# Kernel tuning notes

Hardware: AMD Instinct MI355X
Metric: run time of the kernel (lower is better)

The kernel has to match this reference:

```python
import jax, jax.numpy as jnp
from jax import lax
import numpy as np

EPS = 1e-5

def sign_ste(x):
    # Binarize to {-1,+1} with straight-through estimator (matches BNN Binarize)
    return x + lax.stop_gradient(jnp.where(x >= 0, 1.0, -1.0).astype(x.dtype) - x)

def bn(x, g, b, m, v, axis):
    shp = [1] * x.ndim
    shp[axis] = -1
    inv = g.reshape(shp) / jnp.sqrt(v.reshape(shp) + EPS)
    return (x - m.reshape(shp)) * inv + b.reshape(shp)

def bconv(x, w, b, p):
    # binarized-weight conv, NCHW / OIHW
    y = lax.conv_general_dilated(x, sign_ste(w), (1, 1), [(p, p), (p, p)],
                                 dimension_numbers=('NCHW', 'OIHW', 'NCHW'))
    return y + b[None, :, None, None]

def conv_block(x, w, b, g, bt, m, v, p):
    # BinarizeConv2d -> BatchNorm2d(eval) -> Hardtanh -> Quantizer(1 bit)
    return sign_ste(jnp.clip(bn(bconv(x, w, b, p), g, bt, m, v, 1), -1.0, 1.0))

def maxpool2(x):
    return lax.reduce_window(x, -jnp.inf, lax.max, (1, 1, 2, 2), (1, 1, 2, 2), 'VALID')


def setup_inputs() -> dict:
    key = jax.random.key(0)
    ks = iter(jax.random.split(key, 64))
    B = 4096
    d = {}
    d['x'] = jax.random.normal(next(ks), (B, 1, 28, 28), dtype=jnp.float32)

    def u(shape):
        return jax.random.uniform(next(ks), shape, minval=-1.0, maxval=1.0, dtype=jnp.float32)

    def bn_params(c, pre):
        d[pre + 'g'] = u((c,)) * 0.5 + 1.0
        d[pre + 'bt'] = u((c,)) * 0.1
        d[pre + 'm'] = u((c,)) * 0.1
        d[pre + 'v'] = jax.random.uniform(next(ks), (c,), minval=0.5, maxval=1.5, dtype=jnp.float32)

    # stem conv 1->16, k=3
    d['w1'] = u((16, 1, 3, 3)); d['b1'] = jnp.full((16,), 0.01, jnp.float32); bn_params(16, '')
    d['g1'], d['bt1'], d['m1'], d['v1'] = d.pop('g'), d.pop('bt'), d.pop('m'), d.pop('v')
    # inception branches 16->32 each
    d['wa'] = u((32, 16, 1, 1)); d['ba'] = jnp.full((32,), 0.01, jnp.float32); bn_params(32, 'a_')
    d['wb'] = u((32, 16, 3, 3)); d['bb'] = jnp.full((32,), 0.01, jnp.float32); bn_params(32, 'b_')
    d['wc'] = u((32, 16, 5, 5)); d['bc'] = jnp.full((32,), 0.01, jnp.float32); bn_params(32, 'c_')
    # classifier
    d['wf1'] = u((1024, 7 * 7 * 3 * 32)); d['bf1'] = jnp.full((1024,), 0.01, jnp.float32); bn_params(1024, 'f1_')
    d['wf2'] = u((10, 1024)); d['bf2'] = jnp.full((10,), 0.01, jnp.float32); bn_params(10, 'f2_')
    return d


def reference(x, w1, b1, g1, bt1, m1, v1,
              wa, ba, a_g, a_bt, a_m, a_v,
              wb, bb, b_g, b_bt, b_m, b_v,
              wc, bc, c_g, c_bt, c_m, c_v,
              wf1, bf1, f1_g, f1_bt, f1_m, f1_v,
              wf2, bf2, f2_g, f2_bt, f2_m, f2_v):
    h = conv_block(x, w1, b1, g1, bt1, m1, v1, 1)          # [B,16,28,28]
    h = maxpool2(h)                                         # [B,16,14,14]
    h = sign_ste(h)  # BinarizeConv2d binarizes its input (>1 channel); no-op on +/-1
    ya = conv_block(h, wa, ba, a_g, a_bt, a_m, a_v, 0)
    yb = conv_block(h, wb, bb, b_g, b_bt, b_m, b_v, 1)
    yc = conv_block(h, wc, bc, c_g, c_bt, c_m, c_v, 2)
    h = jnp.concatenate([ya, yb, yc], axis=1)               # [B,96,14,14]
    h = maxpool2(h)                                         # [B,96,7,7]
    h = h.reshape(h.shape[0], -1)                           # [B,4704] (NCHW flatten)
    # fc1: binarized input + binarized weights, BN1d, hardtanh, quantize
    h = sign_ste(h) @ sign_ste(wf1).T + bf1
    h = sign_ste(jnp.clip(bn(h, f1_g, f1_bt, f1_m, f1_v, 1), -1.0, 1.0))
    # dropout is identity in eval mode
    h = sign_ste(h) @ sign_ste(wf2).T + bf2
    h = bn(h, f2_g, f2_bt, f2_m, f2_v, 1)
    return jax.nn.log_softmax(h, axis=-1)                   # [B,10]
```

## Files before the change

kernel.cpp:

```cpp
#include <hip/hip_runtime.h>
#include <stdint.h>

typedef unsigned long long u64;
typedef unsigned int u32;
typedef unsigned short u16;

struct InPtrs { const float* p[37]; };

#define OFF_THR1     0
#define OFF_W1D      128
#define OFF_WREC     1280
#define OFF_SMAXBC   4352
#define OFF_SMAXF1   11008
#define OFF_WF2P     15104
#define OFF_A2       16384
#define OFF_C2       16448
#define OFF_WF1P     16512
#define OFF_H2       622720
#define OFF_HB2      3047552

__device__ __forceinline__ int clampi(int v, int lo, int hi) { return v < lo ? lo : (v > hi ? hi : v); }

__global__ __launch_bounds__(1024) void kprep(InPtrs P, char* __restrict__ ws) {
  const float* w1 = P.p[1]; const float* b1 = P.p[2];
  const float* g1 = P.p[3]; const float* bt1 = P.p[4]; const float* m1 = P.p[5]; const float* v1 = P.p[6];
  const float* wa = P.p[7]; const float* ba = P.p[8];
  const float* ag = P.p[9]; const float* abt = P.p[10]; const float* am = P.p[11]; const float* av = P.p[12];
  const float* wb = P.p[13]; const float* bb = P.p[14];
  const float* bg = P.p[15]; const float* bbt = P.p[16]; const float* bm = P.p[17]; const float* bv = P.p[18];
  const float* wc = P.p[19]; const float* bc = P.p[20];
  const float* bf1 = P.p[26];
  const float* f1g = P.p[27]; const float* f1bt = P.p[28]; const float* f1m = P.p[29]; const float* f1v = P.p[30];
  const float* wf2 = P.p[31]; const float* bf2 = P.p[32];
  const float* cg = P.p[21]; const float* cbt = P.p[22]; const float* cm = P.p[23]; const float* cv = P.p[24];
  const float* f2g = P.p[33]; const float* f2bt = P.p[34]; const float* f2m = P.p[35]; const float* f2v = P.p[36];

  double* thr1 = (double*)(ws + OFF_THR1);
  double* w1d  = (double*)(ws + OFF_W1D);
  u64* wrec = (u64*)(ws + OFF_WREC);
  u64* smaxbc = (u64*)(ws + OFF_SMAXBC);
  int* smf1 = (int*)(ws + OFF_SMAXF1);
  u64* wf2p = (u64*)(ws + OFF_WF2P);
  float* a2 = (float*)(ws + OFF_A2);
  float* c2 = (float*)(ws + OFF_C2);

  __shared__ u64 wbpL[96];
  __shared__ u64 wcpL[256];
  __shared__ double thBL[32], thCL[32];
  __shared__ u32 wamS[32], smaS[32];

  int t = threadIdx.x;
  int wave = t >> 6, lane = t & 63;
  int blk = blockIdx.x;

  if (blk == 0) {
    if (t < 32) {
      u32 m = 0;
      for (int c = 0; c < 16; c++) if (wa[t*16+c] >= 0.f) m |= 1u << c;
      wamS[t] = m;
      double ia = (double)ag[t] / sqrt((double)av[t] + 1e-5);
      double thA = (double)am[t] - (double)abt[t]/ia - (double)ba[t];
      int kmin = (int)ceil(thA);
      int sm = (16 - kmin) >> 1;
      smaS[t] = (u32)clampi(sm + 1, 0, 65535);
      double ib = (double)bg[t] / sqrt((double)bv[t] + 1e-5);
      thBL[t] = (double)bm[t] - (double)bbt[t]/ib - (double)bb[t];
      double ic = (double)cg[t] / sqrt((double)cv[t] + 1e-5);
      thCL[t] = (double)cm[t] - (double)cbt[t]/ic - (double)bc[t];
    }
    for (int w = wave; w < 96; w += 16) {
      int ch = w / 3, k = w - 3*ch;
      int tt = 4*k + (lane >> 4), c = lane & 15;
      bool pred = false;
      if (tt < 9) pred = (wb[ch*144 + c*9 + tt] >= 0.f);
      u64 m = __ballot(pred);
      if (lane == 0) wbpL[w] = m;
    }
    for (int w = wave; w < 256; w += 16) {
      int ch = w >> 3, k = w & 7;
      int tt = 4*k + (lane >> 4), c = lane & 15;
      bool pred = false;
      if (k < 7 && tt < 25) pred = (wc[ch*400 + c*25 + tt] >= 0.f);
      u64 m = __ballot(pred);
      if (lane == 0) wcpL[w] = m;
    }
    __syncthreads();
    if (t < 384) {
      int ch = t / 12, k = t - 12*ch;
      u64 v = 0;
      if (k < 7) v = wcpL[ch*8 + k];
      else if (k < 10) v = wbpL[ch*3 + (k - 7)];
      wrec[ch*12 + k] = v;
    }
    if (t < 800) {
      const int irep[5] = {0, 1, 5, 12, 13};
      int cls = t >> 5, ch = t & 31;
      int rc = cls / 5, cc = cls - 5*rc;
      int ir = irep[rc], jr = irep[cc];
      u64 invC[7] = {0,0,0,0,0,0,0};
      u64 invB[3] = {0,0,0};
      int nInvC = 0, nInvB = 0;
      #pragma unroll
      for (int tt = 0; tt < 25; tt++) {
        int di = tt/5 - 2, dj = tt%5 - 2;
        bool val = (ir+di >= 0 && ir+di < 14 && jr+dj >= 0 && jr+dj < 14);
        if (!val) { invC[tt>>2] |= 0xFFFFull << ((tt&3)*16); nInvC++; }
      }
      #pragma unroll
      for (int tt = 0; tt < 9; tt++) {
        int di = tt/3 - 1, dj = tt%3 - 1;
        bool val = (ir+di >= 0 && ir+di < 14 && jr+dj >= 0 && jr+dj < 14);
        if (!val) { invB[tt>>2] |= 0xFFFFull << ((tt&3)*16); nInvB++; }
      }
      int pinvC = 0;
      #pragma unroll
      for (int k = 0; k < 7; k++) pinvC += __popcll(wcpL[ch*8+k] & invC[k]);
      int pinvB = 0;
      #pragma unroll
      for (int k = 0; k < 3; k++) pinvB += __popcll(wbpL[ch*3+k] & invB[k]);
      int nvC = 16*(25 - nInvC), nvB = 16*(9 - nInvB);
      int kminC = (int)ceil(thCL[ch]);
      int kminB = (int)ceil(thBL[ch]);
      int smC = ((nvC - kminC) >> 1) + pinvC;
      int smB = ((nvB - kminB) >> 1) + pinvB;
      u64 pB = (u64)clampi(smB + 1, 0, 65535);
      u64 pC = (u64)clampi(smC + 1, 0, 65535);
      smaxbc[cls*33 + ch] = ((u64)wamS[ch] << 48) | ((u64)smaS[ch] << 32) | (pB << 16) | pC;
    }
  } else if (blk == 1) {
    for (int w = wave; w < 160; w += 16) {
      int o = w >> 4, kk = w & 15;
      bool pred = (wf2[o*1024 + kk*64 + lane] >= 0.f);
      u64 m = __ballot(pred);
      if (lane == 0) wf2p[w] = m;
    }
  } else if (blk == 2) {
    {
      int o = t;
      double inv = (double)f1g[o] / sqrt((double)f1v[o] + 1e-5);
      double th = (double)f1m[o] - (double)f1bt[o]/inv - (double)bf1[o];
      int kmin = (int)ceil(th);
      smf1[o] = ((4704 - kmin) >> 1) + 1;
    }
    if (t < 10) {
      double inv = (double)f2g[t] / sqrt((double)f2v[t] + 1e-5);
      a2[t] = (float)inv;
      c2[t] = (float)(((double)bf2[t] - (double)f2m[t]) * inv + (double)f2bt[t]);
    }
  } else {
    if (t < 144) w1d[t] = (w1[t] >= 0.f) ? 1.0 : -1.0;
    if (t < 16) {
      double inv = (double)g1[t] / sqrt((double)v1[t] + 1e-5);
      thr1[t] = (double)m1[t] - (double)bt1[t] / inv - (double)b1[t];
    }
  }
}

__global__ __launch_bounds__(256) void kfused(const float* __restrict__ x, const float* __restrict__ wf1,
                                              const char* __restrict__ ws,
                                              u32* __restrict__ h2u32, u64* __restrict__ wf1p) {
  __shared__ float wshF[144];
  __shared__ float thrF[16];
  __shared__ double thrD[16];
  __shared__ u16 hp[324];
  __shared__ u32 rr[196][3];
  __shared__ u64 smbc[825];
  __shared__ __align__(16) u64 wrecL[384];

  int t = threadIdx.x;

  if (blockIdx.x < 1024) {
    unsigned char* flag = (unsigned char*)smbc;
    int o = blockIdx.x;
    const float* row = wf1 + (size_t)o*4704;
    for (int i = t; i < 4704; i += 256) flag[i] = (row[i] >= 0.f);
    __syncthreads();
    int w0 = t >> 6, lane = t & 63;
    for (int w = w0; w < 74; w += 4) {
      int fp = w*64 + lane;
      bool bit = false;
      if (fp < 4704) { int s = fp / 96, c = fp - 96*s; bit = flag[c*49 + s] != 0; }
      u64 m = __ballot(bit);
      if (lane == 0) wf1p[(size_t)o*74 + w] = m;
    }
    return;
  }

  int b = blockIdx.x - 1024;
  const double* w1d  = (const double*)(ws + OFF_W1D);
  const double* thr1 = (const double*)(ws + OFF_THR1);
  const u64* wrec_g = (const u64*)(ws + OFF_WREC);
  const u64* smaxbc_g = (const u64*)(ws + OFF_SMAXBC);

  if (t < 144) wshF[t] = (float)w1d[t];
  else if (t < 160) { thrF[t-144] = (float)thr1[t-144]; thrD[t-144] = thr1[t-144]; }
  for (int i = t; i < 384; i += 256) wrecL[i] = wrec_g[i];
  for (int i = t; i < 825; i += 256) smbc[i] = smaxbc_g[i];
  {
    u32* hp32 = (u32*)hp;
    for (int i = t; i < 162; i += 256) hp32[i] = 0;
  }
  __syncthreads();

  int pi = t / 14, pj = t - 14*pi;
  if (t < 196) {
    const float* xi = x + (size_t)b*784;
    float p[16];
    #pragma unroll
    for (int r = 0; r < 4; r++) {
      int ii = 2*pi - 1 + r;
      #pragma unroll
      for (int c = 0; c < 4; c++) {
        int jj = 2*pj - 1 + c;
        bool v = (ii >= 0 && ii < 28 && jj >= 0 && jj < 28);
        int a = v ? (ii*28 + jj) : 0;
        float f = xi[a];
        p[r*4+c] = v ? f : 0.0f;
      }
    }
    u32 bits = 0;
    for (int o = 0; o < 16; o++) {
      float a00 = 0.f, a01 = 0.f, a10 = 0.f, a11 = 0.f;
      #pragma unroll
      for (int dy = 0; dy < 3; dy++)
        #pragma unroll
        for (int dx = 0; dx < 3; dx++) {
          float w = wshF[o*9 + dy*3 + dx];
          a00 += p[dy*4 + dx]       * w;
          a01 += p[dy*4 + dx + 1]   * w;
          a10 += p[(dy+1)*4 + dx]   * w;
          a11 += p[(dy+1)*4 + dx+1] * w;
        }
      float th = thrF[o];
      float mx = fmaxf(fmaxf(a00, a01), fmaxf(a10, a11));
      bool bit;
      if (fabsf(mx - th) < 5e-4f) {
        double d00 = 0.0, d01 = 0.0, d10 = 0.0, d11 = 0.0;
        #pragma unroll
        for (int dy = 0; dy < 3; dy++)
          #pragma unroll
          for (int dx = 0; dx < 3; dx++) {
            double w = (double)wshF[o*9 + dy*3 + dx];
            d00 += (double)p[dy*4 + dx]       * w;
            d01 += (double)p[dy*4 + dx + 1]   * w;
            d10 += (double)p[(dy+1)*4 + dx]   * w;
            d11 += (double)p[(dy+1)*4 + dx+1] * w;
          }
        double thd = thrD[o];
        bit = (d00 >= thd) || (d01 >= thd) || (d10 >= thd) || (d11 >= thd);
      } else {
        bit = (mx >= th);
      }
      bits |= (u32)bit << o;
    }
    hp[(pi+2)*18 + (pj+2)] = (u16)bits;
  }
  __syncthreads();

  if (t < 196) {
    const u16* hpb = &hp[pi*18 + pj];
    u32 tp[25];
    #pragma unroll
    for (int r = 0; r < 5; r++)
      #pragma unroll
      for (int c = 0; c < 5; c++) tp[r*5+c] = hpb[r*18 + c];
    u32 h0 = tp[12];
    u64 qc[6], qb[2];
    u32 qc6 = tp[24], qb2 = tp[18];
    qc[0] = (u64)tp[0]  | (u64)tp[1]<<16  | (u64)tp[2]<<32  | (u64)tp[3]<<48;
    qc[1] = (u64)tp[4]  | (u64)tp[5]<<16  | (u64)tp[6]<<32  | (u64)tp[7]<<48;
    qc[2] = (u64)tp[8]  | (u64)tp[9]<<16  | (u64)tp[10]<<32 | (u64)tp[11]<<48;
    qc[3] = (u64)tp[12] | (u64)tp[13]<<16 | (u64)tp[14]<<32 | (u64)tp[15]<<48;
    qc[4] = (u64)tp[16] | (u64)tp[17]<<16 | (u64)tp[18]<<32 | (u64)tp[19]<<48;
    qc[5] = (u64)tp[20] | (u64)tp[21]<<16 | (u64)tp[22]<<32 | (u64)tp[23]<<48;
    qb[0] = (u64)tp[6]  | (u64)tp[7]<<16  | (u64)tp[8]<<32  | (u64)tp[11]<<48;
    qb[1] = (u64)tp[12] | (u64)tp[13]<<16 | (u64)tp[16]<<32 | (u64)tp[17]<<48;
    int rc = (pi < 2) ? pi : (pi > 11 ? pi - 9 : 2);
    int cc = (pj < 2) ? pj : (pj > 11 ? pj - 9 : 2);
    const u64* mrow = &smbc[(rc*5 + cc)*33];
    const ulonglong2* R2 = (const ulonglong2*)wrecL;
    u32 r0 = 0, r1 = 0, r2 = 0;
    #pragma unroll 8
    for (int ch = 0; ch < 32; ch++) {
      ulonglong2 w01 = R2[ch*6+0], w23 = R2[ch*6+1], w45 = R2[ch*6+2];
      ulonglong2 w67 = R2[ch*6+3], w89 = R2[ch*6+4];
      u64 meta = mrow[ch];
      int Sc = __popcll(qc[0]^w01.x) + __popcll(qc[1]^w01.y) + __popcll(qc[2]^w23.x)
             + __popcll(qc[3]^w23.y) + __popcll(qc[4]^w45.x) + __popcll(qc[5]^w45.y)
             + __popc(qc6 ^ (u32)w67.x);
      int Sb = __popcll(qb[0]^w67.y) + __popcll(qb[1]^w89.x) + __popc(qb2 ^ (u32)w89.y);
      int Sa = __popc(h0 ^ (u32)(meta >> 48));
      r0 |= (u32)(Sa < (int)((meta >> 32) & 0xFFFFu)) << ch;
      r1 |= (u32)(Sb < (int)((meta >> 16) & 0xFFFFu)) << ch;
      r2 |= (u32)(Sc < (int)(meta & 0xFFFFu)) << ch;
    }
    rr[t][0] = r0; rr[t][1] = r1; rr[t][2] = r2;
  }
  __syncthreads();
  if (t < 148) {
    u32 v = 0;
    if (t < 147) {
      int s = t / 3, qq = t - 3*s;
      int sp = s / 7, sj = s - 7*sp;
      int base = (2*sp)*14 + 2*sj;
      v = rr[base][qq] | rr[base+1][qq] | rr[base+14][qq] | rr[base+15][qq];
    }
    h2u32[(size_t)b*148 + t] = v;
  }
}

__global__ __launch_bounds__(256) void kfc1(const u64* __restrict__ h2, const u64* __restrict__ wf1p,
                                            const int* __restrict__ smf1, u64* __restrict__ hb2) {
  __shared__ __align__(16) u64 aL[64*74];
  __shared__ __align__(16) u64 wL[64*74];
  __shared__ unsigned char bitsb[64][64];
  int bx = blockIdx.x, by = blockIdx.y, t = threadIdx.x;
  const ulonglong2* ga = reinterpret_cast<const ulonglong2*>(h2 + (size_t)by*(64*74));
  ulonglong2* la = reinterpret_cast<ulonglong2*>(aL);
  for (int i = t; i < 64*37; i += 256) la[i] = ga[i];
  const ulonglong2* gw = reinterpret_cast<const ulonglong2*>(wf1p + (size_t)bx*(64*74));
  ulonglong2* lw = reinterpret_cast<ulonglong2*>(wL);
  for (int i = t; i < 64*37; i += 256) {
    int o = i / 37, w2 = i - 37*o;
    int po = ((o & 15) << 2) | (o >> 4);
    lw[po*37 + w2] = gw[i];
  }
  __syncthreads();
  int ig = t & 15, og = t >> 4;
  const ulonglong2* A0 = reinterpret_cast<const ulonglong2*>(aL + (ig     )*74);
  const ulonglong2* A1 = reinterpret_cast<const ulonglong2*>(aL + (ig + 16)*74);
  const ulonglong2* A2 = reinterpret_cast<const ulonglong2*>(aL + (ig + 32)*74);
  const ulonglong2* A3 = reinterpret_cast<const ulonglong2*>(aL + (ig + 48)*74);
  const ulonglong2* W0 = reinterpret_cast<const ulonglong2*>(wL + (og*4 + 0)*74);
  const ulonglong2* W1 = reinterpret_cast<const ulonglong2*>(wL + (og*4 + 1)*74);
  const ulonglong2* W2 = reinterpret_cast<const ulonglong2*>(wL + (og*4 + 2)*74);
  const ulonglong2* W3 = reinterpret_cast<const ulonglong2*>(wL + (og*4 + 3)*74);
  int s[4][4];
  #pragma unroll
  for (int i = 0; i < 4; i++)
    #pragma unroll
    for (int j = 0; j < 4; j++) s[i][j] = 0;
  for (int w = 0; w < 37; w++) {
    ulonglong2 b0 = W0[w], b1 = W1[w], b2 = W2[w], b3 = W3[w];
    ulonglong2 a;
    a = A0[w];
    s[0][0] += __popcll(a.x^b0.x)+__popcll(a.y^b0.y); s[0][1] += __popcll(a.x^b1.x)+__popcll(a.y^b1.y);
    s[0][2] += __popcll(a.x^b2.x)+__popcll(a.y^b2.y); s[0][3] += __popcll(a.x^b3.x)+__popcll(a.y^b3.y);
    a = A1[w];
    s[1][0] += __popcll(a.x^b0.x)+__popcll(a.y^b0.y); s[1][1] += __popcll(a.x^b1.x)+__popcll(a.y^b1.y);
    s[1][2] += __popcll(a.x^b2.x)+__popcll(a.y^b2.y); s[1][3] += __popcll(a.x^b3.x)+__popcll(a.y^b3.y);
    a = A2[w];
    s[2][0] += __popcll(a.x^b0.x)+__popcll(a.y^b0.y); s[2][1] += __popcll(a.x^b1.x)+__popcll(a.y^b1.y);
    s[2][2] += __popcll(a.x^b2.x)+__popcll(a.y^b2.y); s[2][3] += __popcll(a.x^b3.x)+__popcll(a.y^b3.y);
    a = A3[w];
    s[3][0] += __popcll(a.x^b0.x)+__popcll(a.y^b0.y); s[3][1] += __popcll(a.x^b1.x)+__popcll(a.y^b1.y);
    s[3][2] += __popcll(a.x^b2.x)+__popcll(a.y^b2.y); s[3][3] += __popcll(a.x^b3.x)+__popcll(a.y^b3.y);
  }
  int th0 = smf1[bx*64 + og];
  int th1 = smf1[bx*64 + og + 16];
  int th2 = smf1[bx*64 + og + 32];
  int th3 = smf1[bx*64 + og + 48];
  #pragma unroll
  for (int i = 0; i < 4; i++) {
    int im = ig + 16*i;
    bitsb[im][og     ] = s[i][0] < th0;
    bitsb[im][og + 16] = s[i][1] < th1;
    bitsb[im][og + 32] = s[i][2] < th2;
    bitsb[im][og + 48] = s[i][3] < th3;
  }
  __syncthreads();
  if (t < 64) {
    u64 wd = 0;
    #pragma unroll
    for (int j = 0; j < 64; j++) wd |= (u64)bitsb[t][j] << j;
    hb2[(size_t)(by*64 + t)*16 + bx] = wd;
  }
}

__global__ __launch_bounds__(256) void kfc2(const u64* __restrict__ hb2, const char* __restrict__ ws,
                                            float* __restrict__ out, int B) {
  __shared__ u64 w2[160];
  __shared__ float a2s[10], c2s[10];
  const u64* wf2p = (const u64*)(ws + OFF_WF2P);
  const float* a2 = (const float*)(ws + OFF_A2);
  const float* c2 = (const float*)(ws + OFF_C2);
  int t = threadIdx.x;
  for (int i = t; i < 160; i += 256) w2[i] = wf2p[i];
  if (t < 10) { a2s[t] = a2[t]; c2s[t] = c2[t]; }
  __syncthreads();
  int img = blockIdx.x*256 + t;
  if (img >= B) return;
  u64 a[16];
  #pragma unroll
  for (int w = 0; w < 16; w++) a[w] = hb2[(size_t)img*16 + w];
  float z[10];
  #pragma unroll
  for (int o = 0; o < 10; o++) {
    int S = 0;
    #pragma unroll
    for (int w = 0; w < 16; w++) S += __popcll(a[w] ^ w2[o*16 + w]);
    z[o] = (float)(1024 - 2*S) * a2s[o] + c2s[o];
  }
  float M = z[0];
  #pragma unroll
  for (int o = 1; o < 10; o++) M = fmaxf(M, z[o]);
  float se = 0.f;
  #pragma unroll
  for (int o = 0; o < 10; o++) se += expf(z[o] - M);
  float lse = M + logf(se);
  #pragma unroll
  for (int o = 0; o < 10; o++) out[(size_t)img*10 + o] = z[o] - lse;
}

extern "C" void kernel_launch(void* const* d_in, const int* in_sizes, int n_in,
                              void* d_out, int out_size, void* d_ws, size_t ws_size,
                              hipStream_t stream) {
  int B = in_sizes[0] / 784;
  char* ws = (char*)d_ws;
  InPtrs P;
  for (int i = 0; i < 37; i++) P.p[i] = (const float*)d_in[i];

  kprep<<<4, 1024, 0, stream>>>(P, ws);
  kfused<<<1024 + B, 256, 0, stream>>>((const float*)d_in[0], (const float*)d_in[25], ws,
                                       (u32*)(ws + OFF_H2), (u64*)(ws + OFF_WF1P));
  dim3 g(16, B/64);
  kfc1<<<g, 256, 0, stream>>>((const u64*)(ws + OFF_H2), (const u64*)(ws + OFF_WF1P),
                              (const int*)(ws + OFF_SMAXF1), (u64*)(ws + OFF_HB2));
  kfc2<<<(B + 255)/256, 256, 0, stream>>>((const u64*)(ws + OFF_HB2), ws, (float*)d_out, B);
}
```

Before: 138.7 us.

## Restructure fc1 popcount GEMM: activations in registers, wave-uniform weights from global

The fc1 binary GEMM kernel now stages only the activation tile in LDS, transposed so each lane owns one image, and loads half of that row (37 words) into registers at a time. Weights are read straight from global memory with wave-uniform addresses, which the compiler can turn into scalar loads, so the weight tile no longer goes through shared memory. Each wave handles 16 outputs in groups of 4 over two K halves, keeping partial sums in a small LDS buffer between halves. This is meant to cut LDS traffic and bank conflicts, at the cost of heavy register use (37 u64 values per lane) and reliance on the scalar cache for weight reads.

```diff
diff --git a/kernel.cpp b/kernel.cpp
--- a/kernel.cpp
+++ b/kernel.cpp
@@ -311,62 +311,61 @@
 
 __global__ __launch_bounds__(256) void kfc1(const u64* __restrict__ h2, const u64* __restrict__ wf1p,
                                             const int* __restrict__ smf1, u64* __restrict__ hb2) {
-  __shared__ __align__(16) u64 aL[64*74];
-  __shared__ __align__(16) u64 wL[64*74];
+  __shared__ __align__(16) u64 aT[74*65];
+  __shared__ u16 sums[64][66];
   __shared__ unsigned char bitsb[64][64];
   int bx = blockIdx.x, by = blockIdx.y, t = threadIdx.x;
-  const ulonglong2* ga = reinterpret_cast<const ulonglong2*>(h2 + (size_t)by*(64*74));
-  ulonglong2* la = reinterpret_cast<ulonglong2*>(aL);
-  for (int i = t; i < 64*37; i += 256) la[i] = ga[i];
-  const ulonglong2* gw = reinterpret_cast<const ulonglong2*>(wf1p + (size_t)bx*(64*74));
-  ulonglong2* lw = reinterpret_cast<ulonglong2*>(wL);
-  for (int i = t; i < 64*37; i += 256) {
-    int o = i / 37, w2 = i - 37*o;
-    int po = ((o & 15) << 2) | (o >> 4);
-    lw[po*37 + w2] = gw[i];
-  }
-  __syncthreads();
-  int ig = t & 15, og = t >> 4;
-  const ulonglong2* A0 = reinterpret_cast<const ulonglong2*>(aL + (ig     )*74);
-  const ulonglong2* A1 = reinterpret_cast<const ulonglong2*>(aL + (ig + 16)*74);
-  const ulonglong2* A2 = reinterpret_cast<const ulonglong2*>(aL + (ig + 32)*74);
-  const ulonglong2* A3 = reinterpret_cast<const ulonglong2*>(aL + (ig + 48)*74);
-  const ulonglong2* W0 = reinterpret_cast<const ulonglong2*>(wL + (og*4 + 0)*74);
-  const ulonglong2* W1 = reinterpret_cast<const ulonglong2*>(wL + (og*4 + 1)*74);
-  const ulonglong2* W2 = reinterpret_cast<const ulonglong2*>(wL + (og*4 + 2)*74);
-  const ulonglong2* W3 = reinterpret_cast<const ulonglong2*>(wL + (og*4 + 3)*74);
-  int s[4][4];
-  #pragma unroll
-  for (int i = 0; i < 4; i++)
-    #pragma unroll
-    for (int j = 0; j < 4; j++) s[i][j] = 0;
-  for (int w = 0; w < 37; w++) {
-    ulonglong2 b0 = W0[w], b1 = W1[w], b2 = W2[w], b3 = W3[w];
-    ulonglong2 a;
-    a = A0[w];
-    s[0][0] += __popcll(a.x^b0.x)+__popcll(a.y^b0.y); s[0][1] += __popcll(a.x^b1.x)+__popcll(a.y^b1.y);
-    s[0][2] += __popcll(a.x^b2.x)+__popcll(a.y^b2.y); s[0][3] += __popcll(a.x^b3.x)+__popcll(a.y^b3.y);
-    a = A1[w];
-    s[1][0] += __popcll(a.x^b0.x)+__popcll(a.y^b0.y); s[1][1] += __popcll(a.x^b1.x)+__popcll(a.y^b1.y);
-    s[1][2] += __popcll(a.x^b2.x)+__popcll(a.y^b2.y); s[1][3] += __popcll(a.x^b3.x)+__popcll(a.y^b3.y);
-    a = A2[w];
-    s[2][0] += __popcll(a.x^b0.x)+__popcll(a.y^b0.y); s[2][1] += __popcll(a.x^b1.x)+__popcll(a.y^b1.y);
-    s[2][2] += __popcll(a.x^b2.x)+__popcll(a.y^b2.y); s[2][3] += __popcll(a.x^b3.x)+__popcll(a.y^b3.y);
-    a = A3[w];
-    s[3][0] += __popcll(a.x^b0.x)+__popcll(a.y^b0.y); s[3][1] += __popcll(a.x^b1.x)+__popcll(a.y^b1.y);
-    s[3][2] += __popcll(a.x^b2.x)+__popcll(a.y^b2.y); s[3][3] += __popcll(a.x^b3.x)+__popcll(a.y^b3.y);
-  }
-  int th0 = smf1[bx*64 + og];
-  int th1 = smf1[bx*64 + og + 16];
-  int th2 = smf1[bx*64 + og + 32];
-  int th3 = smf1[bx*64 + og + 48];
-  #pragma unroll
-  for (int i = 0; i < 4; i++) {
-    int im = ig + 16*i;
-    bitsb[im][og     ] = s[i][0] < th0;
-    bitsb[im][og + 16] = s[i][1] < th1;
-    bitsb[im][og + 32] = s[i][2] < th2;
-    bitsb[im][og + 48] = s[i][3] < th3;
+  const u64* ga = h2 + (size_t)by*64*74;
+  for (int i = t; i < 64*74; i += 256) {
+    int img = i / 74, w = i - 74*img;
+    aT[w*65 + img] = ga[i];
+  }
+  __syncthreads();
+  int lane = t & 63;
+  int wv = __builtin_amdgcn_readfirstlane(t >> 6);
+  u64 areg[37];
+  #pragma unroll
+  for (int j = 0; j < 37; j++) areg[j] = aT[j*65 + lane];
+  for (int oq = 0; oq < 4; oq++) {
+    int ob = (wv << 4) + oq*4;
+    const u64* W0 = wf1p + (size_t)(bx*64 + ob + 0)*74;
+    const u64* W1 = wf1p + (size_t)(bx*64 + ob + 1)*74;
+    const u64* W2 = wf1p + (size_t)(bx*64 + ob + 2)*74;
+    const u64* W3 = wf1p + (size_t)(bx*64 + ob + 3)*74;
+    int S0 = 0, S1 = 0, S2 = 0, S3 = 0;
+    #pragma unroll
+    for (int j = 0; j < 37; j++) {
+      u64 a = areg[j];
+      S0 += __popcll(a ^ W0[j]); S1 += __popcll(a ^ W1[j]);
+      S2 += __popcll(a ^ W2[j]); S3 += __popcll(a ^ W3[j]);
+    }
+    sums[lane][ob+0] = (u16)S0; sums[lane][ob+1] = (u16)S1;
+    sums[lane][ob+2] = (u16)S2; sums[lane][ob+3] = (u16)S3;
+  }
+  #pragma unroll
+  for (int j = 0; j < 37; j++) areg[j] = aT[(37 + j)*65 + lane];
+  for (int oq = 0; oq < 4; oq++) {
+    int ob = (wv << 4) + oq*4;
+    const u64* W0 = wf1p + (size_t)(bx*64 + ob + 0)*74 + 37;
+    const u64* W1 = wf1p + (size_t)(bx*64 + ob + 1)*74 + 37;
+    const u64* W2 = wf1p + (size_t)(bx*64 + ob + 2)*74 + 37;
+    const u64* W3 = wf1p + (size_t)(bx*64 + ob + 3)*74 + 37;
+    int S0 = sums[lane][ob+0], S1 = sums[lane][ob+1];
+    int S2 = sums[lane][ob+2], S3 = sums[lane][ob+3];
+    #pragma unroll
+    for (int j = 0; j < 37; j++) {
+      u64 a = areg[j];
+      S0 += __popcll(a ^ W0[j]); S1 += __popcll(a ^ W1[j]);
+      S2 += __popcll(a ^ W2[j]); S3 += __popcll(a ^ W3[j]);
+    }
+    int th0 = smf1[bx*64 + ob + 0];
+    int th1 = smf1[bx*64 + ob + 1];
+    int th2 = smf1[bx*64 + ob + 2];
+    int th3 = smf1[bx*64 + ob + 3];
+    bitsb[lane][ob+0] = S0 < th0;
+    bitsb[lane][ob+1] = S1 < th1;
+    bitsb[lane][ob+2] = S2 < th2;
+    bitsb[lane][ob+3] = S3 < th3;
   }
   __syncthreads();
   if (t < 64) {
```

After: 141.5 us. 1.02x slower.
